# Kernel tuning notes

Hardware: AMD Instinct MI355X
Metric: run time of the kernel (lower is better)

## Reference

```python
import jax, jax.numpy as jnp
import numpy as np

B, V, D, K = 32, 4096, 64, 512


def setup_inputs() -> dict:
    key = jax.random.key(0)
    k1, k2 = jax.random.split(key)
    z_e = jax.random.normal(k1, (B, V, D), dtype=jnp.float32)
    # nn.Embedding weight initialized uniform(-1/K, 1/K)
    emb = jax.random.uniform(k2, (K, D), dtype=jnp.float32, minval=-1.0 / K, maxval=1.0 / K)
    return {"z_e": z_e, "emb": emb}


def reference(z_e, emb):
    b, v, d = z_e.shape
    flat = z_e.reshape(-1, d)  # [N, D], N = B*V
    # Squared Euclidean distances via dot-product expansion.
    # torch.cdist returns sqrt of this, but argmin is identical (monotone sqrt).
    d2 = (
        jnp.sum(flat * flat, axis=-1, keepdims=True)  # [N, 1]
        - 2.0 * flat @ emb.T                          # [N, K]
        + jnp.sum(emb * emb, axis=-1)                 # [K]
    )
    indices = jnp.argmin(d2, axis=1)                  # [N]
    z_q = emb[indices].reshape(z_e.shape)             # [B, V, D]
    z_q_st = z_e + jax.lax.stop_gradient(z_q - z_e)   # straight-through
    return z_q_st, z_q, indices.reshape(b, v)
```

## Files before the change

### kernel.cpp

```cpp
#include <hip/hip_runtime.h>


#define VQ_N (32 * 4096)
#define VQ_D 64
#define VQ_K 512

__device__ __forceinline__ float freeze(float x) {
  asm volatile("" : "+v"(x));
  return x;
}

__global__ __launch_bounds__(256) void vq_norms_kernel(
    const float* __restrict__ emb, float* __restrict__ nrm) {
  int k = blockIdx.x * blockDim.x + threadIdx.x;
  if (k < VQ_K) {
    const float* e = emb + k * VQ_D;
    float r0 = freeze(e[0] * e[0]), r1 = freeze(e[1] * e[1]);
    float r2 = freeze(e[2] * e[2]), r3 = freeze(e[3] * e[3]);
    float r4 = freeze(e[4] * e[4]), r5 = freeze(e[5] * e[5]);
    float r6 = freeze(e[6] * e[6]), r7 = freeze(e[7] * e[7]);
#pragma unroll
    for (int i = 8; i < VQ_D; i += 8) {
      r0 += freeze(e[i + 0] * e[i + 0]); r1 += freeze(e[i + 1] * e[i + 1]);
      r2 += freeze(e[i + 2] * e[i + 2]); r3 += freeze(e[i + 3] * e[i + 3]);
      r4 += freeze(e[i + 4] * e[i + 4]); r5 += freeze(e[i + 5] * e[i + 5]);
      r6 += freeze(e[i + 6] * e[i + 6]); r7 += freeze(e[i + 7] * e[i + 7]);
    }
    nrm[k] = ((r0 + r1) + (r2 + r3)) + ((r4 + r5) + (r6 + r7));
  }
}

__global__ __launch_bounds__(256, 3) void vq_main_kernel(
    const float* __restrict__ z_e, const float* __restrict__ emb,
    const float* __restrict__ nrm, float* __restrict__ out_st,
    float* __restrict__ out_q, float* __restrict__ out_idx) {
  __shared__ float s_val[256];
  __shared__ int s_idx[256];
  __shared__ int s_best[64];

  const int tid = threadIdx.x;
  const int lane = tid & 63;
  const int chunk = __builtin_amdgcn_readfirstlane(tid >> 6);
  const int row = blockIdx.x * 64 + lane;

  float z[VQ_D];
  const float4* z4 = (const float4*)(z_e + (size_t)row * VQ_D);
#pragma unroll
  for (int j = 0; j < 16; ++j) {
    float4 v = z4[j];
    z[4 * j + 0] = v.x; z[4 * j + 1] = v.y;
    z[4 * j + 2] = v.z; z[4 * j + 3] = v.w;
  }

  float r0 = freeze(z[0] * z[0]), r1 = freeze(z[1] * z[1]);
  float r2 = freeze(z[2] * z[2]), r3 = freeze(z[3] * z[3]);
  float r4 = freeze(z[4] * z[4]), r5 = freeze(z[5] * z[5]);
  float r6 = freeze(z[6] * z[6]), r7 = freeze(z[7] * z[7]);
#pragma unroll
  for (int i = 8; i < VQ_D; i += 8) {
    r0 += freeze(z[i + 0] * z[i + 0]); r1 += freeze(z[i + 1] * z[i + 1]);
    r2 += freeze(z[i + 2] * z[i + 2]); r3 += freeze(z[i + 3] * z[i + 3]);
    r4 += freeze(z[i + 4] * z[i + 4]); r5 += freeze(z[i + 5] * z[i + 5]);
    r6 += freeze(z[i + 6] * z[i + 6]); r7 += freeze(z[i + 7] * z[i + 7]);
  }
  const float A = ((r0 + r1) + (r2 + r3)) + ((r4 + r5) + (r6 + r7));

  const int k0 = chunk * (VQ_K / 4);
  float bestv = 3.4e38f;
  int best = k0;
  for (int kk = k0; kk < k0 + VQ_K / 4; kk += 4) {
    const float* e0 = emb + (size_t)(kk + 0) * VQ_D;
    const float* e1 = emb + (size_t)(kk + 1) * VQ_D;
    const float* e2 = emb + (size_t)(kk + 2) * VQ_D;
    const float* e3 = emb + (size_t)(kk + 3) * VQ_D;
    float a0 = 0.f, a1 = 0.f, a2 = 0.f, a3 = 0.f;
#pragma unroll
    for (int d = 0; d < VQ_D; ++d) {
      a0 = fmaf(z[d], e0[d], a0);
      a1 = fmaf(z[d], e1[d], a1);
      a2 = fmaf(z[d], e2[d], a2);
      a3 = fmaf(z[d], e3[d], a3);
    }
    float t0 = fmaf(-2.0f, a0, A) + nrm[kk + 0];
    float t1 = fmaf(-2.0f, a1, A) + nrm[kk + 1];
    float t2 = fmaf(-2.0f, a2, A) + nrm[kk + 2];
    float t3 = fmaf(-2.0f, a3, A) + nrm[kk + 3];
    if (t0 < bestv) { bestv = t0; best = kk + 0; }
    if (t1 < bestv) { bestv = t1; best = kk + 1; }
    if (t2 < bestv) { bestv = t2; best = kk + 2; }
    if (t3 < bestv) { bestv = t3; best = kk + 3; }
  }

  s_val[chunk * 64 + lane] = bestv;
  s_idx[chunk * 64 + lane] = best;
  __syncthreads();

  if (tid < 64) {
    float v = s_val[tid];
    int b = s_idx[tid];
#pragma unroll
    for (int c = 1; c < 4; ++c) {
      float vc = s_val[c * 64 + tid];
      if (vc < v) { v = vc; b = s_idx[c * 64 + tid]; }
    }
    s_best[tid] = b;
    out_idx[row] = (float)b;
  }
  __syncthreads();

  const float4* e4 = (const float4*)emb;
  const size_t base4 = (size_t)blockIdx.x * 64 * 16;
  float4* o0 = (float4*)out_st;
  float4* o1 = (float4*)out_q;
#pragma unroll
  for (int t = 0; t < 4; ++t) {
    int i = t * 256 + tid;
    int r = i >> 4, j = i & 15;
    float4 v = e4[s_best[r] * 16 + j];
    o0[base4 + i] = v;
    o1[base4 + i] = v;
  }
}

extern "C" void kernel_launch(void* const* d_in, const int* in_sizes, int n_in,
                              void* d_out, int out_size, void* d_ws,
                              size_t ws_size, hipStream_t stream) {
  const float* z_e = (const float*)d_in[0];
  const float* emb = (const float*)d_in[1];
  float* nrm = (float*)d_ws;

  float* out_st = (float*)d_out;
  float* out_q = out_st + (size_t)VQ_N * VQ_D;
  float* out_idx = out_q + (size_t)VQ_N * VQ_D;

  vq_norms_kernel<<<(VQ_K + 255) / 256, 256, 0, stream>>>(emb, nrm);
  vq_main_kernel<<<VQ_N / 64, 256, 0, stream>>>(z_e, emb, nrm, out_st, out_q,
                                                out_idx);
}
```

Before: 247.5 us.

## Stage z rows in LDS transposed and widen codebook unroll to eight

Rows of z are no longer held in 64 registers per thread. They are loaded cooperatively with coalesced float4 reads into a transposed LDS tile and read back per dimension chunk. This frees registers so the codebook loop can handle 8 codes per iteration instead of 4, which halves the number of z reads per code. The occupancy hint of 3 in launch bounds is dropped. In exchange the kernel adds LDS reads inside the inner loop, an extra barrier and 16 KB of shared memory per block, and the change in register pressure could alter occupancy.

```diff
diff --git a/kernel.cpp b/kernel.cpp
--- a/kernel.cpp
+++ b/kernel.cpp
@@ -30,10 +30,11 @@
   }
 }
 
-__global__ __launch_bounds__(256, 3) void vq_main_kernel(
+__global__ __launch_bounds__(256) void vq_main_kernel(
     const float* __restrict__ z_e, const float* __restrict__ emb,
     const float* __restrict__ nrm, float* __restrict__ out_st,
     float* __restrict__ out_q, float* __restrict__ out_idx) {
+  __shared__ float4 z_lds[16][64];
   __shared__ float s_val[256];
   __shared__ int s_idx[256];
   __shared__ int s_best[64];
@@ -41,54 +42,85 @@
   const int tid = threadIdx.x;
   const int lane = tid & 63;
   const int chunk = __builtin_amdgcn_readfirstlane(tid >> 6);
-  const int row = blockIdx.x * 64 + lane;
+  const int row0 = blockIdx.x * 64;
+  const int row = row0 + lane;
 
-  float z[VQ_D];
-  const float4* z4 = (const float4*)(z_e + (size_t)row * VQ_D);
+  const float4* zg = (const float4*)(z_e + (size_t)row0 * VQ_D);
 #pragma unroll
-  for (int j = 0; j < 16; ++j) {
-    float4 v = z4[j];
-    z[4 * j + 0] = v.x; z[4 * j + 1] = v.y;
-    z[4 * j + 2] = v.z; z[4 * j + 3] = v.w;
+  for (int t = 0; t < 4; ++t) {
+    int i = t * 256 + tid;
+    z_lds[i & 15][i >> 4] = zg[i];
   }
+  __syncthreads();
 
-  float r0 = freeze(z[0] * z[0]), r1 = freeze(z[1] * z[1]);
-  float r2 = freeze(z[2] * z[2]), r3 = freeze(z[3] * z[3]);
-  float r4 = freeze(z[4] * z[4]), r5 = freeze(z[5] * z[5]);
-  float r6 = freeze(z[6] * z[6]), r7 = freeze(z[7] * z[7]);
+  float r0, r1, r2, r3, r4, r5, r6, r7;
+  {
+    float4 p0 = z_lds[0][lane], p1 = z_lds[1][lane];
+    r0 = freeze(p0.x * p0.x); r1 = freeze(p0.y * p0.y);
+    r2 = freeze(p0.z * p0.z); r3 = freeze(p0.w * p0.w);
+    r4 = freeze(p1.x * p1.x); r5 = freeze(p1.y * p1.y);
+    r6 = freeze(p1.z * p1.z); r7 = freeze(p1.w * p1.w);
 #pragma unroll
-  for (int i = 8; i < VQ_D; i += 8) {
-    r0 += freeze(z[i + 0] * z[i + 0]); r1 += freeze(z[i + 1] * z[i + 1]);
-    r2 += freeze(z[i + 2] * z[i + 2]); r3 += freeze(z[i + 3] * z[i + 3]);
-    r4 += freeze(z[i + 4] * z[i + 4]); r5 += freeze(z[i + 5] * z[i + 5]);
-    r6 += freeze(z[i + 6] * z[i + 6]); r7 += freeze(z[i + 7] * z[i + 7]);
+    for (int c = 2; c < 16; c += 2) {
+      float4 q0 = z_lds[c][lane], q1 = z_lds[c + 1][lane];
+      r0 += freeze(q0.x * q0.x); r1 += freeze(q0.y * q0.y);
+      r2 += freeze(q0.z * q0.z); r3 += freeze(q0.w * q0.w);
+      r4 += freeze(q1.x * q1.x); r5 += freeze(q1.y * q1.y);
+      r6 += freeze(q1.z * q1.z); r7 += freeze(q1.w * q1.w);
+    }
   }
   const float A = ((r0 + r1) + (r2 + r3)) + ((r4 + r5) + (r6 + r7));
 
   const int k0 = chunk * (VQ_K / 4);
   float bestv = 3.4e38f;
   int best = k0;
-  for (int kk = k0; kk < k0 + VQ_K / 4; kk += 4) {
+  for (int kk = k0; kk < k0 + VQ_K / 4; kk += 8) {
     const float* e0 = emb + (size_t)(kk + 0) * VQ_D;
     const float* e1 = emb + (size_t)(kk + 1) * VQ_D;
     const float* e2 = emb + (size_t)(kk + 2) * VQ_D;
     const float* e3 = emb + (size_t)(kk + 3) * VQ_D;
+    const float* e4 = emb + (size_t)(kk + 4) * VQ_D;
+    const float* e5 = emb + (size_t)(kk + 5) * VQ_D;
+    const float* e6 = emb + (size_t)(kk + 6) * VQ_D;
+    const float* e7 = emb + (size_t)(kk + 7) * VQ_D;
     float a0 = 0.f, a1 = 0.f, a2 = 0.f, a3 = 0.f;
+    float a4 = 0.f, a5 = 0.f, a6 = 0.f, a7 = 0.f;
 #pragma unroll
-    for (int d = 0; d < VQ_D; ++d) {
-      a0 = fmaf(z[d], e0[d], a0);
-      a1 = fmaf(z[d], e1[d], a1);
-      a2 = fmaf(z[d], e2[d], a2);
-      a3 = fmaf(z[d], e3[d], a3);
+    for (int c = 0; c < 16; ++c) {
+      float4 zc = z_lds[c][lane];
+      a0 = fmaf(zc.x, e0[4 * c + 0], a0); a0 = fmaf(zc.y, e0[4 * c + 1], a0);
+      a0 = fmaf(zc.z, e0[4 * c + 2], a0); a0 = fmaf(zc.w, e0[4 * c + 3], a0);
+      a1 = fmaf(zc.x, e1[4 * c + 0], a1); a1 = fmaf(zc.y, e1[4 * c + 1], a1);
+      a1 = fmaf(zc.z, e1[4 * c + 2], a1); a1 = fmaf(zc.w, e1[4 * c + 3], a1);
+      a2 = fmaf(zc.x, e2[4 * c + 0], a2); a2 = fmaf(zc.y, e2[4 * c + 1], a2);
+      a2 = fmaf(zc.z, e2[4 * c + 2], a2); a2 = fmaf(zc.w, e2[4 * c + 3], a2);
+      a3 = fmaf(zc.x, e3[4 * c + 0], a3); a3 = fmaf(zc.y, e3[4 * c + 1], a3);
+      a3 = fmaf(zc.z, e3[4 * c + 2], a3); a3 = fmaf(zc.w, e3[4 * c + 3], a3);
+      a4 = fmaf(zc.x, e4[4 * c + 0], a4); a4 = fmaf(zc.y, e4[4 * c + 1], a4);
+      a4 = fmaf(zc.z, e4[4 * c + 2], a4); a4 = fmaf(zc.w, e4[4 * c + 3], a4);
+      a5 = fmaf(zc.x, e5[4 * c + 0], a5); a5 = fmaf(zc.y, e5[4 * c + 1], a5);
+      a5 = fmaf(zc.z, e5[4 * c + 2], a5); a5 = fmaf(zc.w, e5[4 * c + 3], a5);
+      a6 = fmaf(zc.x, e6[4 * c + 0], a6); a6 = fmaf(zc.y, e6[4 * c + 1], a6);
+      a6 = fmaf(zc.z, e6[4 * c + 2], a6); a6 = fmaf(zc.w, e6[4 * c + 3], a6);
+      a7 = fmaf(zc.x, e7[4 * c + 0], a7); a7 = fmaf(zc.y, e7[4 * c + 1], a7);
+      a7 = fmaf(zc.z, e7[4 * c + 2], a7); a7 = fmaf(zc.w, e7[4 * c + 3], a7);
     }
     float t0 = fmaf(-2.0f, a0, A) + nrm[kk + 0];
     float t1 = fmaf(-2.0f, a1, A) + nrm[kk + 1];
     float t2 = fmaf(-2.0f, a2, A) + nrm[kk + 2];
     float t3 = fmaf(-2.0f, a3, A) + nrm[kk + 3];
+    float t4 = fmaf(-2.0f, a4, A) + nrm[kk + 4];
+    float t5 = fmaf(-2.0f, a5, A) + nrm[kk + 5];
+    float t6 = fmaf(-2.0f, a6, A) + nrm[kk + 6];
+    float t7 = fmaf(-2.0f, a7, A) + nrm[kk + 7];
     if (t0 < bestv) { bestv = t0; best = kk + 0; }
     if (t1 < bestv) { bestv = t1; best = kk + 1; }
     if (t2 < bestv) { bestv = t2; best = kk + 2; }
     if (t3 < bestv) { bestv = t3; best = kk + 3; }
+    if (t4 < bestv) { bestv = t4; best = kk + 4; }
+    if (t5 < bestv) { bestv = t5; best = kk + 5; }
+    if (t6 < bestv) { bestv = t6; best = kk + 6; }
+    if (t7 < bestv) { bestv = t7; best = kk + 7; }
   }
 
   s_val[chunk * 64 + lane] = bestv;
@@ -108,7 +140,7 @@
   }
   __syncthreads();
 
-  const float4* e4 = (const float4*)emb;
+  const float4* eg4 = (const float4*)emb;
   const size_t base4 = (size_t)blockIdx.x * 64 * 16;
   float4* o0 = (float4*)out_st;
   float4* o1 = (float4*)out_q;
@@ -116,7 +148,7 @@
   for (int t = 0; t < 4; ++t) {
     int i = t * 256 + tid;
     int r = i >> 4, j = i & 15;
-    float4 v = e4[s_best[r] * 16 + j];
+    float4 v = eg4[s_best[r] * 16 + j];
     o0[base4 + i] = v;
     o1[base4 + i] = v;
   }
```

New measurement: 237.4 us. 4.1% less time.
